# Performance work log

Measured on AMD Instinct MI355X. Metric: run time of the kernel, lower is better.

The kernel has to match this reference:

```python
import jax, jax.numpy as jnp
import numpy as np

B, T, D = 2, 2048, 2048
H, DH, DR, DL = 16, 128, 64, 512
WINDOW, STRIDE, GLOBAL = 512, 64, 128
BASE, MAX_SEQ, ORIG_MAX = 10000.0, 131072, 4096
BETA_FAST, BETA_SLOW = 32.0, 1.0
SCALE = 1.0 / np.sqrt(DH)
SCALE_ROPE = 1.0 / np.sqrt(DR)


def _yarn_inv_freq():
    base_inv = 1.0 / (BASE ** (np.arange(0, DR, 2, dtype=np.float32) / DR))
    scale = MAX_SEQ / ORIG_MAX
    freqs = np.arange(DR // 2, dtype=np.float32)
    ramp = np.clip((freqs - BETA_SLOW) / (BETA_FAST - BETA_SLOW), 0.0, 1.0)
    return jnp.asarray(base_inv * (1 - ramp) + (base_inv / scale) * ramp)

_INV_FREQ = _yarn_inv_freq()
_YARN_FACTOR = np.float32(0.1 * np.log(MAX_SEQ / ORIG_MAX) + 1.0)


def _apply_rope(x):
    # x: [B, H, T, DR]
    t = jnp.arange(x.shape[2], dtype=jnp.float32)
    fr = t[:, None] * _INV_FREQ[None, :]            # [T, DR/2]
    emb = jnp.concatenate([fr, fr], axis=-1)        # [T, DR]
    cos, sin = jnp.cos(emb), jnp.sin(emb)
    x1, x2 = jnp.split(x, 2, axis=-1)
    rot = jnp.concatenate([-x2, x1], axis=-1)
    return (x * cos + rot * sin) * _YARN_FACTOR


def _sparse_mask(seq_len):
    pos = jnp.arange(seq_len)
    qp, kp = pos[:, None], pos[None, :]
    dist = qp - kp
    half = WINDOW // 2
    window = (dist >= -half) & (dist <= half)
    dilated = (kp % STRIDE == 0) | (kp < GLOBAL)
    causal = kp <= qp
    return (window | dilated) & causal              # [T, T] bool


def setup_inputs() -> dict:
    key = jax.random.key(0)
    ks = jax.random.split(key, 9)
    s = 0.02
    return {
        "x": jax.random.normal(ks[0], (B, T, D), jnp.float32),
        "w_q": jax.random.normal(ks[1], (D, D), jnp.float32) * s,
        "w_dkv": jax.random.normal(ks[2], (D, DL), jnp.float32) * s,
        "w_uk": jax.random.normal(ks[3], (DL, D), jnp.float32) * s,
        "w_uv": jax.random.normal(ks[4], (DL, D), jnp.float32) * s,
        "w_q_pos": jax.random.normal(ks[5], (D, H * DR), jnp.float32) * s,
        "w_k_pos": jax.random.normal(ks[6], (D, H * DR), jnp.float32) * s,
        "w_o": jax.random.normal(ks[7], (D, D), jnp.float32) * s,
    }


def reference(x, w_q, w_dkv, w_uk, w_uv, w_q_pos, w_k_pos, w_o):
    b, t, _ = x.shape
    # MLA projections
    q_c = (x @ w_q).reshape(b, t, H, DH).transpose(0, 2, 1, 3)      # [B,H,T,DH]
    c_kv = x @ w_dkv                                                # [B,T,DL]
    k_c = (c_kv @ w_uk).reshape(b, t, H, DH).transpose(0, 2, 1, 3)
    v_c = (c_kv @ w_uv).reshape(b, t, H, DH).transpose(0, 2, 1, 3)
    # decoupled RoPE branch (YaRN)
    q_r = (x @ w_q_pos).reshape(b, t, H, DR).transpose(0, 2, 1, 3)
    k_r = (x @ w_k_pos).reshape(b, t, H, DR).transpose(0, 2, 1, 3)
    q_r = _apply_rope(q_r)
    k_r = _apply_rope(k_r)
    # combined content + positional scores
    scores = jnp.einsum("bhqd,bhkd->bhqk", q_c, k_c) * SCALE \
           + jnp.einsum("bhqr,bhkr->bhqk", q_r, k_r) * SCALE_ROPE
    mask = _sparse_mask(t)                                          # [T,T]
    scores = jnp.where(mask[None, None], scores, -jnp.inf)
    attn = jax.nn.softmax(scores, axis=-1)
    out = jnp.einsum("bhqk,bhkd->bhqd", attn, v_c)                  # [B,H,T,DH]
    out = out.transpose(0, 2, 1, 3).reshape(b, t, D)
    return out @ w_o
```

## Files before the change

kernel.cpp:

```cpp
#include <hip/hip_runtime.h>
#include <hip/hip_bf16.h>
#include <cstdint>

typedef __attribute__((ext_vector_type(8))) short short8_t;
typedef __attribute__((ext_vector_type(4))) short short4_t;
typedef __attribute__((ext_vector_type(4))) float f32x4_t;

#define AS1 __attribute__((address_space(1)))
#define AS3 __attribute__((address_space(3)))

__device__ __forceinline__ void gload_lds16(const void* g, void* l) {
  __builtin_amdgcn_global_load_lds((const AS1 void*)g, (AS3 void*)l, 16, 0, 0);
}

__device__ __forceinline__ short8_t ld8(const __hip_bfloat16* p) {
  return *(const short8_t*)p;
}

__global__ __launch_bounds__(256) void k_convert(const float* __restrict__ in,
                                                 __hip_bfloat16* __restrict__ out, int n) {
  int i = (blockIdx.x * 256 + threadIdx.x) * 8;
  if (i >= n) return;
  union { short8_t v; __hip_bfloat16 h[8]; } u;
#pragma unroll
  for (int j = 0; j < 8; ++j) u.h[j] = __float2bfloat16(in[i + j]);
  *(short8_t*)(out + i) = u.v;
}

__global__ __launch_bounds__(256) void k_transpose(const float* __restrict__ in,
                                                   __hip_bfloat16* __restrict__ out,
                                                   int R, int C) {
  __shared__ float t[64][65];
  int nct = C >> 6;
  int ct = blockIdx.x % nct, rt = blockIdx.x / nct;
  int r0 = rt << 6, c0 = ct << 6;
#pragma unroll
  for (int i = 0; i < 16; ++i) {
    int idx = i * 256 + threadIdx.x;
    int r = idx >> 6, c = idx & 63;
    t[r][c] = in[(size_t)(r0 + r) * C + c0 + c];
  }
  __syncthreads();
#pragma unroll
  for (int i = 0; i < 16; ++i) {
    int idx = i * 256 + threadIdx.x;
    int c = idx >> 6, r = idx & 63;
    out[(size_t)(c0 + c) * R + r0 + r] = __float2bfloat16(t[r][c]);
  }
}

template<int MODE>
__global__ __launch_bounds__(256) void k_gemm2(const __hip_bfloat16* __restrict__ A,
                                               const __hip_bfloat16* __restrict__ Bt,
                                               int K, int nbx,
                                               void* __restrict__ O0, void* __restrict__ O1,
                                               void* __restrict__ O2, void* __restrict__ O3,
                                               float alpha) {
  __shared__ __align__(16) __hip_bfloat16 Al[4][128 * 32];
  __shared__ __align__(16) __hip_bfloat16 Bl[4][128 * 32];
  int q = gridDim.x >> 3;
  int id = blockIdx.x;
  int sid = (id & 7) * q + (id >> 3);
  int bx = sid % nbx, by = sid / nbx;
  int tid = threadIdx.x, lane = tid & 63, w = tid >> 6;
  int L = lane & 15, hi = lane >> 4;
  int wr = (w >> 1) << 6, wc = (w & 1) << 6;
  f32x4_t acc[4][4] = {};
  const __hip_bfloat16* Ag = A + (size_t)(by * 128) * K;
  const __hip_bfloat16* Bg = Bt + (size_t)(bx * 128) * K;
  int rA = w * 16 + (lane >> 2);
  int cA = (lane & 3) * 8;
  int NT = K >> 5;

  auto stage = [&](int s) {
    int j = s & 3;
    int k0 = s << 5;
    gload_lds16(Ag + (size_t)rA * K + k0 + cA,        &Al[j][(w * 16) * 32]);
    gload_lds16(Ag + (size_t)(rA + 64) * K + k0 + cA, &Al[j][(64 + w * 16) * 32]);
    gload_lds16(Bg + (size_t)rA * K + k0 + cA,        &Bl[j][(w * 16) * 32]);
    gload_lds16(Bg + (size_t)(rA + 64) * K + k0 + cA, &Bl[j][(64 + w * 16) * 32]);
  };

  stage(0); stage(1); stage(2);
  asm volatile("s_waitcnt vmcnt(8)\ns_barrier" ::: "memory");

  for (int t = 0; t < NT; ++t) {
    int j = t & 3;
    short8_t af[4], bf[4];
#pragma unroll
    for (int m = 0; m < 4; ++m) af[m] = ld8(&Al[j][(wr + 16 * m + L) * 32 + 8 * hi]);
#pragma unroll
    for (int n = 0; n < 4; ++n) bf[n] = ld8(&Bl[j][(wc + 16 * n + L) * 32 + 8 * hi]);
    int rem = NT - t;
    if (rem >= 4) stage(t + 3);
    __builtin_amdgcn_s_setprio(1);
#pragma unroll
    for (int m = 0; m < 4; ++m)
#pragma unroll
      for (int n = 0; n < 4; ++n)
        acc[m][n] = __builtin_amdgcn_mfma_f32_16x16x32_bf16(af[m], bf[n], acc[m][n], 0, 0, 0);
    __builtin_amdgcn_s_setprio(0);
    if (rem >= 4)      asm volatile("s_waitcnt vmcnt(8)\ns_barrier" ::: "memory");
    else if (rem == 3) asm volatile("s_waitcnt vmcnt(4)\ns_barrier" ::: "memory");
    else if (rem == 2) asm volatile("s_waitcnt vmcnt(0)\ns_barrier" ::: "memory");
  }

  int r0 = by * 128 + wr + 4 * hi;
  int cb = bx * 128 + wc;

  if (MODE == 1) {
    float* C = (float*)O0;
    size_t N = (size_t)nbx << 7;
#pragma unroll
    for (int m = 0; m < 4; ++m)
#pragma unroll
      for (int n = 0; n < 4; ++n)
#pragma unroll
        for (int i = 0; i < 4; ++i)
          C[(size_t)(r0 + 16 * m + i) * N + cb + 16 * n + L] = acc[m][n][i] * alpha;
  } else if (MODE == 2) {
    __hip_bfloat16* qcb = (__hip_bfloat16*)O0;
    __hip_bfloat16* qrb = (__hip_bfloat16*)O1;
    __hip_bfloat16* krb = (__hip_bfloat16*)O2;
    __hip_bfloat16* ckv = (__hip_bfloat16*)O3;
    if (bx < 16) {
      const float SCALE = 0.08838834764831845f;
#pragma unroll
      for (int m = 0; m < 4; ++m)
#pragma unroll
        for (int n = 0; n < 4; ++n)
#pragma unroll
          for (int i = 0; i < 4; ++i)
            qcb[(size_t)(r0 + 16 * m + i) * 2048 + cb + 16 * n + L] =
                __float2bfloat16(acc[m][n][i] * SCALE);
    } else if (bx < 32) {
      bool isq = bx < 24;
      __hip_bfloat16* dst = isq ? qrb : krb;
      float osc = isq ? 0.16832169878499666f : 1.3465735902799727f;
      int cbl = cb - (isq ? 2048 : 3072);
      float invf[2];
#pragma unroll
      for (int p = 0; p < 2; ++p) {
        float fi = (float)(16 * p + L);
        float bi = __expf(fi * -0.28782313662425574f);
        float ramp = fminf(fmaxf((fi - 1.0f) * (1.0f / 31.0f), 0.0f), 1.0f);
        invf[p] = bi * (1.0f - ramp * (31.0f / 32.0f));
      }
#pragma unroll
      for (int m = 0; m < 4; ++m)
#pragma unroll
        for (int i = 0; i < 4; ++i) {
          int row = r0 + 16 * m + i;
          float ft = (float)(row & 2047);
#pragma unroll
          for (int p = 0; p < 2; ++p) {
            float sn, cs;
            __sincosf(ft * invf[p], &sn, &cs);
            float x1 = acc[m][p][i], x2 = acc[m][p + 2][i];
            dst[(size_t)row * 1024 + cbl + 16 * p + L] =
                __float2bfloat16((x1 * cs - x2 * sn) * osc);
            dst[(size_t)row * 1024 + cbl + 32 + 16 * p + L] =
                __float2bfloat16((x2 * cs + x1 * sn) * osc);
          }
        }
    } else {
      int cbl = cb - 4096;
#pragma unroll
      for (int m = 0; m < 4; ++m)
#pragma unroll
        for (int n = 0; n < 4; ++n)
#pragma unroll
          for (int i = 0; i < 4; ++i)
            ckv[(size_t)(r0 + 16 * m + i) * 512 + cbl + 16 * n + L] =
                __float2bfloat16(acc[m][n][i]);
    }
  } else if (MODE == 3) {
    __hip_bfloat16* kcb = (__hip_bfloat16*)O0;
    __hip_bfloat16* vcb = (__hip_bfloat16*)O1;
    __hip_bfloat16* vT  = (__hip_bfloat16*)O2;
    if (bx < 16) {
#pragma unroll
      for (int m = 0; m < 4; ++m)
#pragma unroll
        for (int n = 0; n < 4; ++n)
#pragma unroll
          for (int i = 0; i < 4; ++i)
            kcb[(size_t)(r0 + 16 * m + i) * 2048 + cb + 16 * n + L] =
                __float2bfloat16(acc[m][n][i]);
    } else {
#pragma unroll
      for (int m = 0; m < 4; ++m)
#pragma unroll
        for (int n = 0; n < 4; ++n) {
          int vcol = cb - 2048 + 16 * n + L;
          int hh = vcol >> 7, dh = vcol & 127;
          int row0 = r0 + 16 * m;
          int b = row0 >> 11, t0 = row0 & 2047;
          union { short4_t v; __hip_bfloat16 h4[4]; } pk;
#pragma unroll
          for (int i = 0; i < 4; ++i) {
            __hip_bfloat16 bv = __float2bfloat16(acc[m][n][i]);
            vcb[(size_t)(row0 + i) * 2048 + vcol] = bv;
            pk.h4[i] = bv;
          }
          *(short4_t*)(vT + ((size_t)((b * 16 + hh) * 128 + dh) * 2048 + t0)) = pk.v;
        }
    }
  }
}

__global__ __launch_bounds__(256) void k_attn(const __hip_bfloat16* __restrict__ qc,
                                              const __hip_bfloat16* __restrict__ kc,
                                              const __hip_bfloat16* __restrict__ vcb,
                                              const __hip_bfloat16* __restrict__ qr,
                                              const __hip_bfloat16* __restrict__ kr,
                                              const __hip_bfloat16* __restrict__ vT,
                                              __hip_bfloat16* __restrict__ ao) {
  const int T = 2048;
  int bid = blockIdx.x;
  int xcd = bid & 7, r = bid >> 3;
  int j = r >> 5, qt = r & 31;
  int bh = xcd + 8 * j;
  int b = bh >> 4, h = bh & 15;
  int tid = threadIdx.x, lane = tid & 63, w = tid >> 6;
  int L = lane & 15, hi = lane >> 4;
  int q0 = qt * 64;

  __shared__ __align__(16) __hip_bfloat16 Kl[64 * 200];
  __shared__ __align__(16) __hip_bfloat16 Vt[128 * 64];
  __shared__ __align__(16) __hip_bfloat16 Pl[4][16 * 72];

  char* Vtb = (char*)Vt;
  const __hip_bfloat16* vTb = vT + (size_t)(b * 16 + h) * 128 * 2048;

  int qrow = q0 + w * 16 + L;
  size_t qb = (size_t)b * T + qrow;
  short8_t qf[6];
#pragma unroll
  for (int c = 0; c < 4; ++c)
    qf[c] = ld8(qc + qb * 2048 + h * 128 + 32 * c + 8 * hi);
#pragma unroll
  for (int c = 0; c < 2; ++c)
    qf[4 + c] = ld8(qr + qb * 1024 + h * 64 + 32 * c + 8 * hi);

  f32x4_t oacc[8] = {};
  float mrow[4], lrow[4];
#pragma unroll
  for (int i = 0; i < 4; ++i) { mrow[i] = -1e30f; lrow[i] = 0.0f; }

  int nd = qt - 6;

  for (int step = 0; step <= qt + 1; ++step) {
    bool compact = (step == qt + 1);
    if (compact && nd <= 0) break;
    int kt = step;
    if (!compact && kt > 1 && kt < qt - 4) continue;
    int k0 = kt * 64;

    if (!compact) {
#pragma unroll
      for (int i = 0; i < 6; ++i) {
        int ch = i * 256 + tid;
        int rr = ch / 24;
        int d = (ch % 24) * 8;
        size_t krow = (size_t)b * T + k0 + rr;
        const __hip_bfloat16* src = (d < 128)
            ? kc + krow * 2048 + h * 128 + d
            : kr + krow * 1024 + h * 64 + (d - 128);
        *(short8_t*)(Kl + rr * 200 + d) = ld8(src);
      }
#pragma unroll
      for (int i = 0; i < 4; ++i) {
        int ch = i * 256 + tid;
        int row = ch >> 3, c = ch & 7;
        int swc = c ^ (row & 7);
        *(short8_t*)(Vtb + row * 128 + 16 * swc) = ld8(vTb + (size_t)row * 2048 + k0 + c * 8);
      }
    } else {
#pragma unroll
      for (int i = 0; i < 6; ++i) {
        int ch = i * 256 + tid;
        int rr = ch / 24;
        int d = (ch % 24) * 8;
        int srcr = (rr < nd) ? 64 * (2 + rr) : 0;
        size_t krow = (size_t)b * T + srcr;
        const __hip_bfloat16* src = (d < 128)
            ? kc + krow * 2048 + h * 128 + d
            : kr + krow * 1024 + h * 64 + (d - 128);
        *(short8_t*)(Kl + rr * 200 + d) = ld8(src);
      }
#pragma unroll
      for (int i = 0; i < 2; ++i) {
        int ch = i * 256 + tid;
        int jj = ch >> 4, d0 = (ch & 15) * 8;
        if (jj < nd) {
          union { short8_t v; __hip_bfloat16 hh[8]; } u;
          u.v = ld8(vcb + (size_t)(b * 2048 + 64 * (2 + jj)) * 2048 + h * 128 + d0);
#pragma unroll
          for (int qq = 0; qq < 8; ++qq) {
            int dh = d0 + qq;
            int swc = (jj >> 3) ^ (dh & 7);
            *(__hip_bfloat16*)(Vtb + dh * 128 + 16 * swc + 2 * (jj & 7)) = u.hh[qq];
          }
        }
      }
    }
    __syncthreads();

    f32x4_t sacc[4] = {};
    __builtin_amdgcn_s_setprio(1);
#pragma unroll
    for (int n = 0; n < 4; ++n)
#pragma unroll
      for (int c = 0; c < 6; ++c) {
        short8_t bfr = ld8(Kl + (16 * n + L) * 200 + 32 * c + 8 * hi);
        sacc[n] = __builtin_amdgcn_mfma_f32_16x16x32_bf16(qf[c], bfr, sacc[n], 0, 0, 0);
      }
    __builtin_amdgcn_s_setprio(0);

    int rbase = q0 + w * 16 + 4 * hi;
    float p[4][4];
    float mt[4];
#pragma unroll
    for (int i = 0; i < 4; ++i) mt[i] = -1e30f;
#pragma unroll
    for (int n = 0; n < 4; ++n) {
      int col = L + 16 * n;
      int k = k0 + col;
#pragma unroll
      for (int i = 0; i < 4; ++i) {
        int rq = rbase + i;
        bool ok = compact ? (col < nd)
                          : ((k <= rq) && ((rq - k <= 256) || ((k & 63) == 0) || (k < 128)));
        float s = ok ? sacc[n][i] : -1e30f;
        p[n][i] = s;
        mt[i] = fmaxf(mt[i], s);
      }
    }
    for (int d = 1; d < 16; d <<= 1)
#pragma unroll
      for (int i = 0; i < 4; ++i) mt[i] = fmaxf(mt[i], __shfl_xor(mt[i], d, 64));
    float al[4], rs[4];
#pragma unroll
    for (int i = 0; i < 4; ++i) {
      float mnew = fmaxf(mrow[i], mt[i]);
      al[i] = __expf(mrow[i] - mnew);
      mrow[i] = mnew;
      rs[i] = 0.0f;
    }
#pragma unroll
    for (int n = 0; n < 4; ++n)
#pragma unroll
      for (int i = 0; i < 4; ++i) {
        float e = __expf(p[n][i] - mrow[i]);
        p[n][i] = e;
        rs[i] += e;
      }
    for (int d = 1; d < 16; d <<= 1)
#pragma unroll
      for (int i = 0; i < 4; ++i) rs[i] += __shfl_xor(rs[i], d, 64);
#pragma unroll
    for (int i = 0; i < 4; ++i) lrow[i] = lrow[i] * al[i] + rs[i];
#pragma unroll
    for (int n = 0; n < 8; ++n)
#pragma unroll
      for (int i = 0; i < 4; ++i) oacc[n][i] *= al[i];

#pragma unroll
    for (int n = 0; n < 4; ++n)
#pragma unroll
      for (int i = 0; i < 4; ++i)
        Pl[w][(4 * hi + i) * 72 + 16 * n + L] = __float2bfloat16(p[n][i]);
    __syncthreads();

    __builtin_amdgcn_s_setprio(1);
#pragma unroll
    for (int ks = 0; ks < 2; ++ks) {
      short8_t pa = ld8(Pl[w] + L * 72 + 32 * ks + 8 * hi);
#pragma unroll
      for (int n = 0; n < 8; ++n) {
        int vrow = 16 * n + L;
        int chunk = (4 * ks + hi) ^ (vrow & 7);
        short8_t bv = *(const short8_t*)(Vtb + vrow * 128 + 16 * chunk);
        oacc[n] = __builtin_amdgcn_mfma_f32_16x16x32_bf16(pa, bv, oacc[n], 0, 0, 0);
      }
    }
    __builtin_amdgcn_s_setprio(0);
    __syncthreads();
  }

#pragma unroll
  for (int n = 0; n < 8; ++n)
#pragma unroll
    for (int i = 0; i < 4; ++i) {
      int rq = q0 + w * 16 + 4 * hi + i;
      int cdh = 16 * n + L;
      float v = oacc[n][i] / lrow[i];
      ao[((size_t)b * T + rq) * 2048 + h * 128 + cdh] = __float2bfloat16(v);
    }
}

extern "C" void kernel_launch(void* const* d_in, const int* in_sizes, int n_in,
                              void* d_out, int out_size, void* d_ws, size_t ws_size,
                              hipStream_t stream) {
  const float* x     = (const float*)d_in[0];
  const float* w_q   = (const float*)d_in[1];
  const float* w_dkv = (const float*)d_in[2];
  const float* w_uk  = (const float*)d_in[3];
  const float* w_uv  = (const float*)d_in[4];
  const float* w_qp  = (const float*)d_in[5];
  const float* w_kp  = (const float*)d_in[6];
  const float* w_o   = (const float*)d_in[7];
  float* out = (float*)d_out;

  char* ws = (char*)d_ws;
  size_t off = 0;
  auto alloc = [&](size_t elems) {
    __hip_bfloat16* p = (__hip_bfloat16*)(ws + off);
    off += ((elems * 2 + 255) & ~(size_t)255);
    return p;
  };
  __hip_bfloat16* xb  = alloc(8388608);
  __hip_bfloat16* Bt1 = alloc(4608UL * 2048);
  __hip_bfloat16* Bt2 = alloc(4096UL * 512);
  __hip_bfloat16* woT = alloc(4194304);
  __hip_bfloat16* qcb = alloc(8388608);
  __hip_bfloat16* ckv = alloc(2097152);
  __hip_bfloat16* kcb = alloc(8388608);
  __hip_bfloat16* vcb = alloc(8388608);
  __hip_bfloat16* qrb = alloc(4194304);
  __hip_bfloat16* krb = alloc(4194304);
  __hip_bfloat16* aob = alloc(8388608);
  __hip_bfloat16* vT  = alloc(8388608);

  k_convert<<<4096, 256, 0, stream>>>(x, xb, 8388608);
  k_transpose<<<32 * 32, 256, 0, stream>>>(w_q,   Bt1,                 2048, 2048);
  k_transpose<<<32 * 16, 256, 0, stream>>>(w_qp,  Bt1 + 2048UL * 2048, 2048, 1024);
  k_transpose<<<32 * 16, 256, 0, stream>>>(w_kp,  Bt1 + 3072UL * 2048, 2048, 1024);
  k_transpose<<<32 * 8,  256, 0, stream>>>(w_dkv, Bt1 + 4096UL * 2048, 2048, 512);
  k_transpose<<<8 * 32,  256, 0, stream>>>(w_uk,  Bt2,                 512, 2048);
  k_transpose<<<8 * 32,  256, 0, stream>>>(w_uv,  Bt2 + 2048UL * 512,  512, 2048);
  k_transpose<<<32 * 32, 256, 0, stream>>>(w_o,   woT,                 2048, 2048);

  k_gemm2<2><<<36 * 32, 256, 0, stream>>>(xb, Bt1, 2048, 36, qcb, qrb, krb, ckv, 1.0f);
  k_gemm2<3><<<32 * 32, 256, 0, stream>>>(ckv, Bt2, 512, 32, kcb, vcb, vT, nullptr, 1.0f);

  k_attn<<<1024, 256, 0, stream>>>(qcb, kcb, vcb, qrb, krb, vT, aob);

  k_gemm2<1><<<16 * 32, 256, 0, stream>>>(aob, woT, 2048, 16, out, nullptr, nullptr, nullptr, 1.0f);
}
```

Measured before the change: 302.1 us.

## Merge prep kernels, swizzle GEMM LDS reads, shrink pipeline to three stages

```diff
diff --git a/kernel.cpp b/kernel.cpp
--- a/kernel.cpp
+++ b/kernel.cpp
@@ -17,22 +17,35 @@
   return *(const short8_t*)p;
 }
 
-__global__ __launch_bounds__(256) void k_convert(const float* __restrict__ in,
-                                                 __hip_bfloat16* __restrict__ out, int n) {
-  int i = (blockIdx.x * 256 + threadIdx.x) * 8;
-  if (i >= n) return;
-  union { short8_t v; __hip_bfloat16 h[8]; } u;
-#pragma unroll
-  for (int j = 0; j < 8; ++j) u.h[j] = __float2bfloat16(in[i + j]);
-  *(short8_t*)(out + i) = u.v;
-}
-
-__global__ __launch_bounds__(256) void k_transpose(const float* __restrict__ in,
-                                                   __hip_bfloat16* __restrict__ out,
-                                                   int R, int C) {
+__global__ __launch_bounds__(256) void k_prep(
+    const float* __restrict__ x, __hip_bfloat16* __restrict__ xb,
+    const float* __restrict__ wq,  const float* __restrict__ wqp,
+    const float* __restrict__ wkp, const float* __restrict__ wdkv,
+    const float* __restrict__ wuk, const float* __restrict__ wuv,
+    const float* __restrict__ wo,
+    __hip_bfloat16* __restrict__ Bt1, __hip_bfloat16* __restrict__ Bt2,
+    __hip_bfloat16* __restrict__ woT) {
   __shared__ float t[64][65];
+  int bid = blockIdx.x;
+  if (bid < 4096) {
+    int i = (bid * 256 + threadIdx.x) * 8;
+    union { short8_t v; __hip_bfloat16 h[8]; } u;
+#pragma unroll
+    for (int j = 0; j < 8; ++j) u.h[j] = __float2bfloat16(x[i + j]);
+    *(short8_t*)(xb + i) = u.v;
+    return;
+  }
+  bid -= 4096;
+  const float* in; __hip_bfloat16* out; int R, C, tile;
+  if (bid < 1024)      { in = wq;   out = Bt1;                 R = 2048; C = 2048; tile = bid; }
+  else if (bid < 1536) { in = wqp;  out = Bt1 + 2048UL * 2048; R = 2048; C = 1024; tile = bid - 1024; }
+  else if (bid < 2048) { in = wkp;  out = Bt1 + 3072UL * 2048; R = 2048; C = 1024; tile = bid - 1536; }
+  else if (bid < 2304) { in = wdkv; out = Bt1 + 4096UL * 2048; R = 2048; C = 512;  tile = bid - 2048; }
+  else if (bid < 2560) { in = wuk;  out = Bt2;                 R = 512;  C = 2048; tile = bid - 2304; }
+  else if (bid < 2816) { in = wuv;  out = Bt2 + 2048UL * 512;  R = 512;  C = 2048; tile = bid - 2560; }
+  else                 { in = wo;   out = woT;                 R = 2048; C = 2048; tile = bid - 2816; }
   int nct = C >> 6;
-  int ct = blockIdx.x % nct, rt = blockIdx.x / nct;
+  int ct = tile % nct, rt = tile / nct;
   int r0 = rt << 6, c0 = ct << 6;
 #pragma unroll
   for (int i = 0; i < 16; ++i) {
@@ -56,12 +69,9 @@
                                                void* __restrict__ O0, void* __restrict__ O1,
                                                void* __restrict__ O2, void* __restrict__ O3,
                                                float alpha) {
-  __shared__ __align__(16) __hip_bfloat16 Al[4][128 * 32];
-  __shared__ __align__(16) __hip_bfloat16 Bl[4][128 * 32];
-  int q = gridDim.x >> 3;
-  int id = blockIdx.x;
-  int sid = (id & 7) * q + (id >> 3);
-  int bx = sid % nbx, by = sid / nbx;
+  __shared__ __align__(16) __hip_bfloat16 Al[3][128 * 32];
+  __shared__ __align__(16) __hip_bfloat16 Bl[3][128 * 32];
+  int bx = blockIdx.x % nbx, by = blockIdx.x / nbx;
   int tid = threadIdx.x, lane = tid & 63, w = tid >> 6;
   int L = lane & 15, hi = lane >> 4;
   int wr = (w >> 1) << 6, wc = (w & 1) << 6;
@@ -69,11 +79,11 @@
   const __hip_bfloat16* Ag = A + (size_t)(by * 128) * K;
   const __hip_bfloat16* Bg = Bt + (size_t)(bx * 128) * K;
   int rA = w * 16 + (lane >> 2);
-  int cA = (lane & 3) * 8;
+  int cA = ((lane & 3) ^ ((lane >> 3) & 3)) * 8;
   int NT = K >> 5;
 
   auto stage = [&](int s) {
-    int j = s & 3;
+    int j = s % 3;
     int k0 = s << 5;
     gload_lds16(Ag + (size_t)rA * K + k0 + cA,        &Al[j][(w * 16) * 32]);
     gload_lds16(Ag + (size_t)(rA + 64) * K + k0 + cA, &Al[j][(64 + w * 16) * 32]);
@@ -81,18 +91,18 @@
     gload_lds16(Bg + (size_t)(rA + 64) * K + k0 + cA, &Bl[j][(64 + w * 16) * 32]);
   };
 
-  stage(0); stage(1); stage(2);
-  asm volatile("s_waitcnt vmcnt(8)\ns_barrier" ::: "memory");
-
+  stage(0); stage(1);
+  asm volatile("s_waitcnt vmcnt(4)\ns_barrier" ::: "memory");
+
+  int hs = hi ^ ((L >> 1) & 3);
   for (int t = 0; t < NT; ++t) {
-    int j = t & 3;
+    int j = t % 3;
     short8_t af[4], bf[4];
 #pragma unroll
-    for (int m = 0; m < 4; ++m) af[m] = ld8(&Al[j][(wr + 16 * m + L) * 32 + 8 * hi]);
-#pragma unroll
-    for (int n = 0; n < 4; ++n) bf[n] = ld8(&Bl[j][(wc + 16 * n + L) * 32 + 8 * hi]);
-    int rem = NT - t;
-    if (rem >= 4) stage(t + 3);
+    for (int m = 0; m < 4; ++m) af[m] = ld8(&Al[j][(wr + 16 * m + L) * 32 + 8 * hs]);
+#pragma unroll
+    for (int n = 0; n < 4; ++n) bf[n] = ld8(&Bl[j][(wc + 16 * n + L) * 32 + 8 * hs]);
+    if (t + 2 < NT) stage(t + 2);
     __builtin_amdgcn_s_setprio(1);
 #pragma unroll
     for (int m = 0; m < 4; ++m)
@@ -100,9 +110,8 @@
       for (int n = 0; n < 4; ++n)
         acc[m][n] = __builtin_amdgcn_mfma_f32_16x16x32_bf16(af[m], bf[n], acc[m][n], 0, 0, 0);
     __builtin_amdgcn_s_setprio(0);
-    if (rem >= 4)      asm volatile("s_waitcnt vmcnt(8)\ns_barrier" ::: "memory");
-    else if (rem == 3) asm volatile("s_waitcnt vmcnt(4)\ns_barrier" ::: "memory");
-    else if (rem == 2) asm volatile("s_waitcnt vmcnt(0)\ns_barrier" ::: "memory");
+    if (t + 2 < NT)      asm volatile("s_waitcnt vmcnt(4)\ns_barrier" ::: "memory");
+    else if (t + 1 < NT) asm volatile("s_waitcnt vmcnt(0)\ns_barrier" ::: "memory");
   }
 
   int r0 = by * 128 + wr + 4 * hi;
@@ -433,14 +442,8 @@
   __hip_bfloat16* aob = alloc(8388608);
   __hip_bfloat16* vT  = alloc(8388608);
 
-  k_convert<<<4096, 256, 0, stream>>>(x, xb, 8388608);
-  k_transpose<<<32 * 32, 256, 0, stream>>>(w_q,   Bt1,                 2048, 2048);
-  k_transpose<<<32 * 16, 256, 0, stream>>>(w_qp,  Bt1 + 2048UL * 2048, 2048, 1024);
-  k_transpose<<<32 * 16, 256, 0, stream>>>(w_kp,  Bt1 + 3072UL * 2048, 2048, 1024);
-  k_transpose<<<32 * 8,  256, 0, stream>>>(w_dkv, Bt1 + 4096UL * 2048, 2048, 512);
-  k_transpose<<<8 * 32,  256, 0, stream>>>(w_uk,  Bt2,                 512, 2048);
-  k_transpose<<<8 * 32,  256, 0, stream>>>(w_uv,  Bt2 + 2048UL * 512,  512, 2048);
-  k_transpose<<<32 * 32, 256, 0, stream>>>(w_o,   woT,                 2048, 2048);
+  k_prep<<<7936, 256, 0, stream>>>(x, xb, w_q, w_qp, w_kp, w_dkv, w_uk, w_uv, w_o,
+                                   Bt1, Bt2, woT);
 
   k_gemm2<2><<<36 * 32, 256, 0, stream>>>(xb, Bt1, 2048, 36, qcb, qrb, krb, ckv, 1.0f);
   k_gemm2<3><<<32 * 32, 256, 0, stream>>>(ckv, Bt2, 512, 32, kcb, vcb, vT, nullptr, 1.0f);
```

Result: faster. 268.5 us (-11.1%).
